# Kernel tuning notes

Hardware: AMD Instinct MI355X
Metric: run time of the kernel (lower is better)

## Reference

```python
import jax, jax.numpy as jnp
import numpy as np

B, P, H = 32768, 128, 64

def setup_inputs() -> dict:
    key = jax.random.key(0)
    ks = jax.random.split(key, 6)
    planet_xy = jax.random.normal(ks[0], (B, P, 2), dtype=jnp.float32)
    planet_m = jax.random.uniform(ks[1], (P,), dtype=jnp.float32)
    ast_xy = jax.random.normal(ks[2], (B, 2), dtype=jnp.float32)
    W1 = jax.random.normal(ks[3], (4, H), dtype=jnp.float32) * 0.5
    b1 = jnp.zeros((H,), dtype=jnp.float32)
    W2 = jax.random.normal(ks[4], (H, H), dtype=jnp.float32) * 0.125
    b2 = jnp.zeros((H,), dtype=jnp.float32)
    return {"planet_xy": planet_xy, "planet_m": planet_m, "ast_xy": ast_xy,
            "W1": W1, "b1": b1, "W2": W2, "b2": b2}

def reference(planet_xy, planet_m, ast_xy, W1, b1, W2, b2):
    # d: (B, P, 2) broadcast difference planet - asteroid
    d = planet_xy - ast_xy[:, None, :]
    dist2 = jnp.sum(d * d, axis=-1) + 1e-6            # (B, P)
    invdist = 1.0 / jnp.sqrt(dist2)                   # (B, P)
    m = jnp.broadcast_to(planet_m[None, :], dist2.shape)  # (B, P)
    feats = jnp.concatenate([d, invdist[..., None], m[..., None]], axis=-1)  # (B, P, 4)
    h = jax.nn.relu(jnp.einsum('bpf,fh->bph', feats, W1) + b1)  # (B, P, H)
    msg = jax.nn.relu(jnp.einsum('bph,hk->bpk', h, W2) + b2)    # (B, P, H)
    return msg.sum(axis=1)                             # (B, H)
```

## Files before the change

kernel.cpp:

```cpp
#include <hip/hip_runtime.h>
#include <hip/hip_fp16.h>

#define NP    128
#define NH    64
#define RST   18
#define ITERS 4
#define WPB   4

typedef __attribute__((ext_vector_type(8))) _Float16 f16x8;
typedef __attribute__((ext_vector_type(4))) _Float16 f16x4;
typedef __attribute__((ext_vector_type(2))) __fp16  hf16x2;
typedef __attribute__((ext_vector_type(4))) float f32x4;

union FragK16 { f16x4 v; unsigned int u[2]; };
union FragK32 { f16x8 v; unsigned int u[4]; };

__device__ __forceinline__ unsigned int pack_pkrtz(float a, float b) {
    hf16x2 t = __builtin_amdgcn_cvt_pkrtz(a, b);
    return __builtin_bit_cast(unsigned int, t);
}

__device__ __forceinline__ unsigned int relu2_pk(unsigned int u) {
    hf16x2 h = __builtin_bit_cast(hf16x2, u);
    h = __builtin_elementwise_max(h, (hf16x2)(__fp16)0.f);
    return __builtin_bit_cast(unsigned int, h);
}

__global__ void __launch_bounds__(256, 2) gnn_wave(
    const float* __restrict__ planet_xy,
    const float* __restrict__ planet_m,
    const float* __restrict__ ast_xy,
    const float* __restrict__ W1,
    const float* __restrict__ b1,
    const float* __restrict__ W2,
    const float* __restrict__ b2,
    float* __restrict__ out)
{
    __shared__ float rsum[WPB][64 * RST];

    const int tid  = threadIdx.x;
    const int wv   = tid >> 6;
    const int lane = tid & 63;
    const int q    = lane >> 4;
    const int lm   = lane & 15;
    const bool q0  = (q == 0);
    const bool q1  = (q == 1);

    FragK16 w1f[4];
    #pragma unroll
    for (int mt = 0; mt < 4; mt++) {
        const int m = 16 * mt + lm;
        float wa = W1[0 * NH + m], wb = W1[1 * NH + m];
        float wc = W1[2 * NH + m], wd = W1[3 * NH + m];
        float be = b1[m];
        w1f[mt].u[0] = q0 ? pack_pkrtz(wa, wb) : (q1 ? pack_pkrtz(be, 0.f) : 0u);
        w1f[mt].u[1] = q0 ? pack_pkrtz(wc, wd) : 0u;
    }

    FragK32 w2a[4][2];
    #pragma unroll
    for (int np = 0; np < 4; np++)
        #pragma unroll
        for (int kk = 0; kk < 2; kk++) {
            const int n = 16 * np + lm;
            const int k0 = 32 * kk + 4 * q;
            const int k1 = 32 * kk + 16 + 4 * q;
            w2a[np][kk].u[0] = pack_pkrtz(W2[(k0 + 0) * NH + n], W2[(k0 + 1) * NH + n]);
            w2a[np][kk].u[1] = pack_pkrtz(W2[(k0 + 2) * NH + n], W2[(k0 + 3) * NH + n]);
            w2a[np][kk].u[2] = pack_pkrtz(W2[(k1 + 0) * NH + n], W2[(k1 + 1) * NH + n]);
            w2a[np][kk].u[3] = pack_pkrtz(W2[(k1 + 2) * NH + n], W2[(k1 + 3) * NH + n]);
        }

    f32x4 b2f[4];
    #pragma unroll
    for (int np = 0; np < 4; np++)
        b2f[np] = *(const f32x4*)&b2[16 * np + 4 * q];

    float pmv[8];
    #pragma unroll
    for (int i = 0; i < 8; i++)
        pmv[i] = planet_m[16 * i + lm];

    const unsigned int bf0_const = q1 ? pack_pkrtz(1.f, 0.f) : 0u;
    const f32x4 zf = (f32x4){0.f, 0.f, 0.f, 0.f};

    int b = (blockIdx.x * WPB + wv) * ITERS;

    for (int it = 0; it < ITERS; ++it, ++b) {
        const float2 axy = *(const float2*)&ast_xy[2 * b];
        float2 pxy[8];
        #pragma unroll
        for (int i = 0; i < 8; i++)
            pxy[i] = *(const float2*)&planet_xy[((size_t)b * NP + 16 * i + lm) * 2];

        f32x4 sums[4];
        #pragma unroll
        for (int np = 0; np < 4; np++)
            sums[np] = zf;

        #pragma unroll
        for (int mi = 0; mi < 8; ++mi) {
            float dx = pxy[mi].x - axy.x, dy = pxy[mi].y - axy.y;
            float inv = __builtin_amdgcn_rsqf(fmaf(dx, dx, fmaf(dy, dy, 1e-6f)));
            FragK16 bf;
            bf.u[0] = q0 ? pack_pkrtz(dx, dy)        : bf0_const;
            bf.u[1] = q0 ? pack_pkrtz(inv, pmv[mi])  : 0u;

            FragK16 hb[4];
            #pragma unroll
            for (int mt = 0; mt < 4; mt++) {
                f32x4 c = __builtin_amdgcn_mfma_f32_16x16x16f16(w1f[mt].v, bf.v, zf, 0, 0, 0);
                hb[mt].u[0] = relu2_pk(pack_pkrtz(c[0], c[1]));
                hb[mt].u[1] = relu2_pk(pack_pkrtz(c[2], c[3]));
            }

            FragK32 hB[2];
            #pragma unroll
            for (int kk = 0; kk < 2; kk++) {
                hB[kk].u[0] = hb[2 * kk + 0].u[0];
                hB[kk].u[1] = hb[2 * kk + 0].u[1];
                hB[kk].u[2] = hb[2 * kk + 1].u[0];
                hB[kk].u[3] = hb[2 * kk + 1].u[1];
            }

            #pragma unroll
            for (int np = 0; np < 4; np++) {
                f32x4 acc = __builtin_amdgcn_mfma_f32_16x16x32_f16(w2a[np][0].v, hB[0].v, b2f[np], 0, 0, 0);
                acc = __builtin_amdgcn_mfma_f32_16x16x32_f16(w2a[np][1].v, hB[1].v, acc, 0, 0, 0);
                sums[np] += __builtin_elementwise_max(acc, zf);
            }
        }

        #pragma unroll
        for (int np = 0; np < 4; np++)
            #pragma unroll
            for (int r = 0; r < 4; r++)
                rsum[wv][(16 * np + 4 * q + r) * RST + lm] = sums[np][r];

        float tot = 0.f;
        #pragma unroll
        for (int i = 0; i < 8; i++) {
            float2 v = *(const float2*)&rsum[wv][lane * RST + 2 * i];
            tot += v.x + v.y;
        }
        out[(size_t)b * NH + lane] = tot;
    }
}

extern "C" void kernel_launch(void* const* d_in, const int* in_sizes, int n_in,
                              void* d_out, int out_size, void* d_ws, size_t ws_size,
                              hipStream_t stream) {
    const float* planet_xy = (const float*)d_in[0];
    const float* planet_m  = (const float*)d_in[1];
    const float* ast_xy    = (const float*)d_in[2];
    const float* W1        = (const float*)d_in[3];
    const float* b1        = (const float*)d_in[4];
    const float* W2        = (const float*)d_in[5];
    const float* b2        = (const float*)d_in[6];
    float* outp            = (float*)d_out;

    const int B = in_sizes[2] / 2;
    const int batches_per_block = WPB * ITERS;
    const int grid = (B + batches_per_block - 1) / batches_per_block;

    gnn_wave<<<grid, 256, 0, stream>>>(planet_xy, planet_m, ast_xy, W1, b1, W2, b2, outp);
}
```

Measured before the change: 128.9 us.

## Reduce planet messages with ones-matrix MFMA instead of LDS reduction

Swaps the operand roles in the second-layer MFMA so outputs are laid out planet-major. The sum over planets then becomes a 16x16x16 MFMA against a matrix of ones, accumulated in registers. This removes the shared-memory staging and the per-lane reduction at the end of each batch element, at the cost of one extra MFMA per tile and fp16 rounding of the messages before summation.

```diff
diff --git a/kernel.cpp b/kernel.cpp
--- a/kernel.cpp
+++ b/kernel.cpp
@@ -3,7 +3,6 @@
 
 #define NP    128
 #define NH    64
-#define RST   18
 #define ITERS 4
 #define WPB   4
 
@@ -36,8 +35,6 @@
     const float* __restrict__ b2,
     float* __restrict__ out)
 {
-    __shared__ float rsum[WPB][64 * RST];
-
     const int tid  = threadIdx.x;
     const int wv   = tid >> 6;
     const int lane = tid & 63;
@@ -57,7 +54,7 @@
         w1f[mt].u[1] = q0 ? pack_pkrtz(wc, wd) : 0u;
     }
 
-    FragK32 w2a[4][2];
+    FragK32 w2b[4][2];
     #pragma unroll
     for (int np = 0; np < 4; np++)
         #pragma unroll
@@ -65,16 +62,18 @@
             const int n = 16 * np + lm;
             const int k0 = 32 * kk + 4 * q;
             const int k1 = 32 * kk + 16 + 4 * q;
-            w2a[np][kk].u[0] = pack_pkrtz(W2[(k0 + 0) * NH + n], W2[(k0 + 1) * NH + n]);
-            w2a[np][kk].u[1] = pack_pkrtz(W2[(k0 + 2) * NH + n], W2[(k0 + 3) * NH + n]);
-            w2a[np][kk].u[2] = pack_pkrtz(W2[(k1 + 0) * NH + n], W2[(k1 + 1) * NH + n]);
-            w2a[np][kk].u[3] = pack_pkrtz(W2[(k1 + 2) * NH + n], W2[(k1 + 3) * NH + n]);
+            w2b[np][kk].u[0] = pack_pkrtz(W2[(k0 + 0) * NH + n], W2[(k0 + 1) * NH + n]);
+            w2b[np][kk].u[1] = pack_pkrtz(W2[(k0 + 2) * NH + n], W2[(k0 + 3) * NH + n]);
+            w2b[np][kk].u[2] = pack_pkrtz(W2[(k1 + 0) * NH + n], W2[(k1 + 1) * NH + n]);
+            w2b[np][kk].u[3] = pack_pkrtz(W2[(k1 + 2) * NH + n], W2[(k1 + 3) * NH + n]);
         }
 
     f32x4 b2f[4];
     #pragma unroll
-    for (int np = 0; np < 4; np++)
-        b2f[np] = *(const f32x4*)&b2[16 * np + 4 * q];
+    for (int np = 0; np < 4; np++) {
+        const float bv = b2[16 * np + lm];
+        b2f[np] = (f32x4){bv, bv, bv, bv};
+    }
 
     float pmv[8];
     #pragma unroll
@@ -83,6 +82,10 @@
 
     const unsigned int bf0_const = q1 ? pack_pkrtz(1.f, 0.f) : 0u;
     const f32x4 zf = (f32x4){0.f, 0.f, 0.f, 0.f};
+
+    FragK16 onesA;
+    onesA.u[0] = 0x3C003C00u;
+    onesA.u[1] = 0x3C003C00u;
 
     int b = (blockIdx.x * WPB + wv) * ITERS;
 
@@ -93,10 +96,10 @@
         for (int i = 0; i < 8; i++)
             pxy[i] = *(const float2*)&planet_xy[((size_t)b * NP + 16 * i + lm) * 2];
 
-        f32x4 sums[4];
+        f32x4 redD[4];
         #pragma unroll
         for (int np = 0; np < 4; np++)
-            sums[np] = zf;
+            redD[np] = zf;
 
         #pragma unroll
         for (int mi = 0; mi < 8; ++mi) {
@@ -114,36 +117,32 @@
                 hb[mt].u[1] = relu2_pk(pack_pkrtz(c[2], c[3]));
             }
 
-            FragK32 hB[2];
+            FragK32 hA[2];
             #pragma unroll
             for (int kk = 0; kk < 2; kk++) {
-                hB[kk].u[0] = hb[2 * kk + 0].u[0];
-                hB[kk].u[1] = hb[2 * kk + 0].u[1];
-                hB[kk].u[2] = hb[2 * kk + 1].u[0];
-                hB[kk].u[3] = hb[2 * kk + 1].u[1];
+                hA[kk].u[0] = hb[2 * kk + 0].u[0];
+                hA[kk].u[1] = hb[2 * kk + 0].u[1];
+                hA[kk].u[2] = hb[2 * kk + 1].u[0];
+                hA[kk].u[3] = hb[2 * kk + 1].u[1];
             }
 
             #pragma unroll
             for (int np = 0; np < 4; np++) {
-                f32x4 acc = __builtin_amdgcn_mfma_f32_16x16x32_f16(w2a[np][0].v, hB[0].v, b2f[np], 0, 0, 0);
-                acc = __builtin_amdgcn_mfma_f32_16x16x32_f16(w2a[np][1].v, hB[1].v, acc, 0, 0, 0);
-                sums[np] += __builtin_elementwise_max(acc, zf);
+                f32x4 acc = __builtin_amdgcn_mfma_f32_16x16x32_f16(hA[0].v, w2b[np][0].v, b2f[np], 0, 0, 0);
+                acc = __builtin_amdgcn_mfma_f32_16x16x32_f16(hA[1].v, w2b[np][1].v, acc, 0, 0, 0);
+
+                FragK16 mf;
+                mf.u[0] = relu2_pk(pack_pkrtz(acc[0], acc[1]));
+                mf.u[1] = relu2_pk(pack_pkrtz(acc[2], acc[3]));
+
+                redD[np] = __builtin_amdgcn_mfma_f32_16x16x16f16(onesA.v, mf.v, redD[np], 0, 0, 0);
             }
         }
 
-        #pragma unroll
-        for (int np = 0; np < 4; np++)
-            #pragma unroll
-            for (int r = 0; r < 4; r++)
-                rsum[wv][(16 * np + 4 * q + r) * RST + lm] = sums[np][r];
-
-        float tot = 0.f;
-        #pragma unroll
-        for (int i = 0; i < 8; i++) {
-            float2 v = *(const float2*)&rsum[wv][lane * RST + 2 * i];
-            tot += v.x + v.y;
-        }
-        out[(size_t)b * NH + lane] = tot;
+        float v = q0 ? redD[0][0]
+                : q1 ? redD[1][0]
+                : (q == 2) ? redD[2][0] : redD[3][0];
+        out[(size_t)b * NH + lane] = v;
     }
 }
 
```

Measured after the change: 121.0 us. 6.1% less time.
